# Optimization experiments

Measured on AMD Instinct MI355X. Metric: run time of the kernel, lower is better.

## Reference

```python
import jax, jax.numpy as jnp
import numpy as np

B, C, Ci, H, W = 4, 256, 128, 64, 64  # batch, in_channels, inter_channels, spatial
BN_EPS = 1e-5


def setup_inputs() -> dict:
    key = jax.random.key(0)
    ks = jax.random.split(key, 8)
    s = (2.0 / C) ** 0.5  # kaiming fan_in std for 1x1 conv over C inputs
    return {
        "a": jax.random.normal(ks[0], (B, C, H, W), jnp.float32),
        "b": jax.random.normal(ks[1], (B, C, H, W), jnp.float32),
        "theta_w": jax.random.normal(ks[2], (Ci, C), jnp.float32) * s,
        "theta_b": jnp.zeros((Ci,), jnp.float32),
        "phi_w": jax.random.normal(ks[3], (Ci, C), jnp.float32) * s,
        "phi_b": jnp.zeros((Ci,), jnp.float32),
        "g_w": jax.random.normal(ks[4], (Ci, C), jnp.float32) * s,
        "g_b": jnp.zeros((Ci,), jnp.float32),
        "W_w": jax.random.normal(ks[5], (C, Ci), jnp.float32) * (2.0 / Ci) ** 0.5,
        "bn_gamma": jnp.ones((C,), jnp.float32),
        "bn_beta": jnp.zeros((C,), jnp.float32),
        "bn_mean": jnp.zeros((C,), jnp.float32),
        "bn_var": jnp.ones((C,), jnp.float32),
    }


def _conv1x1(x, w, bias=None):
    # x: [B,Cin,H,W], w: [Cout,Cin] -> [B,Cout,H,W]
    y = jnp.einsum("oc,bchw->bohw", w, x)
    if bias is not None:
        y = y + bias[None, :, None, None]
    return y


def reference(a, b, theta_w, theta_b, phi_w, phi_b, g_w, g_b, W_w,
              bn_gamma, bn_beta, bn_mean, bn_var):
    Bsz, _, h, w = a.shape
    n = h * w
    theta_a = _conv1x1(a, theta_w, theta_b).reshape(Bsz, Ci, n).transpose(0, 2, 1)  # [B,N,Ci]
    phi_b_ = _conv1x1(b, phi_w, phi_b).reshape(Bsz, Ci, n)                          # [B,Ci,N]
    f = jnp.einsum("bnc,bcm->bnm", theta_a, phi_b_) / n                             # [B,N,N]
    g_b_ = _conv1x1(b, g_w, g_b).reshape(Bsz, Ci, n).transpose(0, 2, 1)             # [B,N,Ci]
    y = jnp.einsum("bnm,bmc->bnc", f, g_b_)                                         # [B,N,Ci]
    y = y.transpose(0, 2, 1).reshape(Bsz, Ci, h, w)
    wy = _conv1x1(y, W_w)                                                           # no bias
    inv = jax.lax.rsqrt(bn_var + BN_EPS)
    out = (wy - bn_mean[None, :, None, None]) * (bn_gamma * inv)[None, :, None, None] \
          + bn_beta[None, :, None, None]
    return out
```

## Files before the change

kernel.cpp:

```cpp
#include <hip/hip_runtime.h>
#include <hip/hip_bf16.h>

#define NSP 4096
#define CCH 256
#define CIN 128
#define BN_EPS 1e-5f

typedef __bf16 bf16x8 __attribute__((ext_vector_type(8)));
typedef __bf16 bf16x4 __attribute__((ext_vector_type(4)));
typedef float f32x4 __attribute__((ext_vector_type(4)));
typedef unsigned short u16x8 __attribute__((ext_vector_type(8)));


__device__ __forceinline__ float4 fetch_tr(const float* __restrict__ A, int lda, int m0,
                                           int k0, int tid) {
  const int r = tid >> 2, kq = (tid & 3) << 2;
  return *(const float4*)(A + (size_t)(m0 + r) * lda + k0 + kq);
}
__device__ __forceinline__ void stash_tr(float (*As)[68], float4 v, int tid) {
  const int r = tid >> 2, kq = (tid & 3) << 2;
  As[kq + 0][r] = v.x; As[kq + 1][r] = v.y; As[kq + 2][r] = v.z; As[kq + 3][r] = v.w;
}
__device__ __forceinline__ float4 fetch_dir(const float* __restrict__ B, int ldb, int k0,
                                            int n0, int tid) {
  const int kr = tid >> 4, nq = (tid & 15) << 2;
  return *(const float4*)(B + (size_t)(k0 + kr) * ldb + n0 + nq);
}
__device__ __forceinline__ void stash_dir(float (*Bs)[68], float4 v, int tid) {
  const int kr = tid >> 4, nq = (tid & 15) << 2;
  *(float4*)(&Bs[kr][nq]) = v;
}

__device__ __forceinline__ void mm16(const float (*As)[68], const float (*Bs)[68],
                                     float acc[4][4], int ty, int tx) {
#pragma unroll
  for (int kk = 0; kk < 16; ++kk) {
    const float4 av = *(const float4*)(&As[kk][ty << 2]);
    const float4 bv = *(const float4*)(&Bs[kk][tx << 2]);
    const float ar[4] = {av.x, av.y, av.z, av.w};
    const float br[4] = {bv.x, bv.y, bv.z, bv.w};
#pragma unroll
    for (int i = 0; i < 4; ++i)
#pragma unroll
      for (int j = 0; j < 4; ++j) acc[i][j] += ar[i] * br[j];
  }
}

__device__ __forceinline__ float wave_reduce(float v) {
#pragma unroll
  for (int off = 32; off; off >>= 1) v += __shfl_down(v, off);
  return v;
}

__device__ __forceinline__ void f8_hilo(const float* __restrict__ p,
                                        bf16x8& h, bf16x8& l) {
  const float4 v0 = *(const float4*)p;
  const float4 v1 = *(const float4*)(p + 4);
  const float vv[8] = {v0.x, v0.y, v0.z, v0.w, v1.x, v1.y, v1.z, v1.w};
  u16x8 hu, lu;
#pragma unroll
  for (int e = 0; e < 8; ++e) {
    const unsigned u = __float_as_uint(vv[e]);
    hu[e] = (unsigned short)(u >> 16);
    const float hf = __uint_as_float(u & 0xffff0000u);
    lu[e] = (unsigned short)(__float_as_uint(vv[e] - hf) >> 16);
  }
  h = *(bf16x8*)&hu;
  l = *(bf16x8*)&lu;
}

__global__ __launch_bounds__(256) void front_kernel(
    const float* __restrict__ bin, const float* __restrict__ a,
    const float* __restrict__ W_w, const float* __restrict__ g_w,
    const float* __restrict__ phi_w, const float* __restrict__ theta_w,
    const float* __restrict__ phi_b, const float* __restrict__ theta_b,
    const float* __restrict__ g_b,
    float* __restrict__ Gpart, float* __restrict__ srow,
    float* __restrict__ Wg, __bf16* __restrict__ Wghi, __bf16* __restrict__ Wglo,
    __bf16* __restrict__ PTthi, __bf16* __restrict__ PTtlo,
    __bf16* __restrict__ at,
    float* __restrict__ vb_g, float* __restrict__ vpt, float* __restrict__ wgb,
    float* __restrict__ dvec) {
  __shared__ float smem[64 * 68];
  const int idx = blockIdx.x;
  const int t = threadIdx.x;
  const int wave = t >> 6, lane = t & 63;
  if (idx < 1024) {
    const int jt = idx & 3, it = (idx >> 2) & 3;
    const int z = idx >> 4, batch = z >> 4, kc = z & 15;
    const int m = lane & 15, q = lane >> 4;
    const float* base = bin + (size_t)batch * CCH * NSP;
    const float* arow = base + (size_t)(it * 64 + wave * 16 + m) * NSP + kc * 256 + q * 8;
    const float* brow = base + (size_t)(jt * 64 + m) * NSP + kc * 256 + q * 8;
    f32x4 acc[4] = {};
#pragma unroll
    for (int ks = 0; ks < 8; ++ks) {
      const int k = ks * 32;
      bf16x8 ah, al;
      f8_hilo(arow + k, ah, al);
#pragma unroll
      for (int t4 = 0; t4 < 4; ++t4) {
        bf16x8 bh, bl;
        f8_hilo(brow + (size_t)t4 * 16 * NSP + k, bh, bl);
        acc[t4] = __builtin_amdgcn_mfma_f32_16x16x32_bf16(ah, bh, acc[t4], 0, 0, 0);
        acc[t4] = __builtin_amdgcn_mfma_f32_16x16x32_bf16(ah, bl, acc[t4], 0, 0, 0);
        acc[t4] = __builtin_amdgcn_mfma_f32_16x16x32_bf16(al, bh, acc[t4], 0, 0, 0);
      }
    }
    float* Gp = Gpart + ((size_t)(kc * 4 + batch)) * 65536;
#pragma unroll
    for (int t4 = 0; t4 < 4; ++t4)
#pragma unroll
      for (int r = 0; r < 4; ++r)
        Gp[(size_t)(it * 64 + wave * 16 + q * 4 + r) * 256 + jt * 64 + t4 * 16 + m] =
            acc[t4][r];
  } else if (idx < 2048) {
    const int p = idx - 1024;
    const int n0 = (p & 63) * 64, c0 = ((p >> 6) & 3) * 64, b = p >> 8;
    float (*tile)[68] = (float(*)[68])smem;
    const int cr = t >> 4, nq = (t & 15) << 2;
    const float* src = a + ((size_t)(b * CCH + c0)) * NSP + n0;
#pragma unroll
    for (int s = 0; s < 4; ++s) {
      const float4 v = *(const float4*)(src + (size_t)(cr + s * 16) * NSP + nq);
      *(float4*)&tile[cr + s * 16][nq] = v;
    }
    __syncthreads();
    const int n = t >> 2, cq = (t & 3) << 4;
    __bf16 outv[16];
#pragma unroll
    for (int i = 0; i < 16; ++i) outv[i] = (__bf16)tile[cq + i][n];
    __bf16* dst = at + ((size_t)(b * NSP + n0 + n)) * CCH + c0 + cq;
    *(bf16x8*)dst = *(bf16x8*)&outv[0];
    *(bf16x8*)(dst + 8) = *(bf16x8*)&outv[8];
  } else if (idx < 3072) {
    const int row = idx - 2048;
    const float* src = bin + (size_t)row * NSP + t * 16;
    float sum = 0.f;
#pragma unroll
    for (int i = 0; i < 4; ++i) {
      const float4 v = *(const float4*)(src + i * 4);
      sum += v.x + v.y + v.z + v.w;
    }
#pragma unroll
    for (int off = 32; off; off >>= 1) sum += __shfl_down(sum, off);
    if ((t & 63) == 0) smem[t >> 6] = sum;
    __syncthreads();
    if (t == 0) srow[row] = smem[0] + smem[1] + smem[2] + smem[3];
  } else if (idx < 3104) {
    const int p = idx - 3072;
    const int zsel = p >> 4, rem = p & 15;
    const int m0 = (rem >> 2) * 64, n0 = (rem & 3) * 64;
    float (*As)[68] = (float(*)[68])smem;
    float (*Bs)[68] = (float(*)[68])(smem + 16 * 68);
    const int ty = t >> 4, tx = t & 15;
    float acc[4][4] = {};
    if (zsel == 0) {
      float4 ar = fetch_tr(W_w, CIN, m0, 0, t);
      float4 br = fetch_dir(g_w, CCH, 0, n0, t);
      for (int kt = 0; kt < 8; ++kt) {
        stash_tr(As, ar, t); stash_dir(Bs, br, t);
        __syncthreads();
        if (kt < 7) { ar = fetch_tr(W_w, CIN, m0, (kt + 1) * 16, t);
                      br = fetch_dir(g_w, CCH, (kt + 1) * 16, n0, t); }
        mm16(As, Bs, acc, ty, tx);
        __syncthreads();
      }
#pragma unroll
      for (int i = 0; i < 4; ++i) {
        const size_t off = (size_t)(m0 + (ty << 2) + i) * 256 + n0 + (tx << 2);
        *(float4*)(Wg + off) = make_float4(acc[i][0], acc[i][1], acc[i][2], acc[i][3]);
        __bf16 h4[4], l4[4];
#pragma unroll
        for (int j = 0; j < 4; ++j) {
          const __bf16 h = (__bf16)acc[i][j];
          h4[j] = h; l4[j] = (__bf16)(acc[i][j] - (float)h);
        }
        *(bf16x4*)(Wghi + off) = *(bf16x4*)h4;
        *(bf16x4*)(Wglo + off) = *(bf16x4*)l4;
      }
    } else {
      float4 ar = fetch_dir(theta_w, CCH, 0, m0, t);
      float4 br = fetch_dir(phi_w, CCH, 0, n0, t);
      for (int kt = 0; kt < 8; ++kt) {
        stash_dir(As, ar, t); stash_dir(Bs, br, t);
        __syncthreads();
        if (kt < 7) { ar = fetch_dir(theta_w, CCH, (kt + 1) * 16, m0, t);
                      br = fetch_dir(phi_w, CCH, (kt + 1) * 16, n0, t); }
        mm16(As, Bs, acc, ty, tx);
        __syncthreads();
      }
#pragma unroll
      for (int i = 0; i < 4; ++i) {
        const size_t off = (size_t)(m0 + (ty << 2) + i) * 256 + n0 + (tx << 2);
        __bf16 h4[4], l4[4];
#pragma unroll
        for (int j = 0; j < 4; ++j) {
          const __bf16 h = (__bf16)acc[i][j];
          h4[j] = h; l4[j] = (__bf16)(acc[i][j] - (float)h);
        }
        *(bf16x4*)(PTthi + off) = *(bf16x4*)h4;
        *(bf16x4*)(PTtlo + off) = *(bf16x4*)l4;
      }
    }
  } else if (idx == 3104) {
    float* tb_s = smem;
    float* pb_s = smem + 128;
    if (t < 128) { tb_s[t] = theta_b[t]; pb_s[t] = phi_b[t]; }
    __syncthreads();
    float acc = 0.f;
#pragma unroll 8
    for (int i = 0; i < 128; ++i) acc += phi_w[(size_t)i * 256 + t] * tb_s[i];
    vb_g[t] = acc;
    if (t < 64) {
      float pv = pb_s[t] * tb_s[t] + pb_s[t + 64] * tb_s[t + 64];
      pv = wave_reduce(pv);
      if (t == 0) dvec[0] = pv;
    }
  } else if (idx == 3105) {
    float* pb_s = smem;
    if (t < 128) pb_s[t] = phi_b[t];
    __syncthreads();
    float acc = 0.f;
#pragma unroll 8
    for (int i = 0; i < 128; ++i) acc += pb_s[i] * theta_w[(size_t)i * 256 + t];
    vpt[t] = acc;
  } else {
    const int p = idx - 3106;
    float* gb_s = smem;
    if (t < 128) gb_s[t] = g_b[t];
    __syncthreads();
    const float2 gv = *(const float2*)&gb_s[lane * 2];
    for (int i = 0; i < 16; ++i) {
      const int o = p * 64 + wave * 16 + i;
      const float2 r = *(const float2*)(W_w + (size_t)o * 128 + lane * 2);
      float v = fmaf(r.x, gv.x, r.y * gv.y);
      v = wave_reduce(v);
      if (lane == 0) wgb[o] = v;
    }
  }
}

__global__ __launch_bounds__(256) void redw2_kernel(
    const float* __restrict__ Gpart, const float* __restrict__ vb_g,
    float* __restrict__ t2_g, const float* __restrict__ srow,
    const float* __restrict__ Wg,
    const __bf16* __restrict__ Wghi, const __bf16* __restrict__ Wglo,
    const __bf16* __restrict__ PTthi, const __bf16* __restrict__ PTtlo,
    __bf16* __restrict__ W2hi, __bf16* __restrict__ W2lo,
    float* __restrict__ Wgs, float* __restrict__ sPTv, float* __restrict__ dvec) {
  const int blk = blockIdx.x;
  const int t = threadIdx.x;
  const int wave = t >> 6, lane = t & 63;
  __shared__ __bf16 Gsh[16][264], Gsl[16][264];
  __shared__ float lds[256];
  if (blk < 256) {
    const int b = blk >> 6, rem = blk & 63;
    const int nt = rem >> 2, mt4 = rem & 3;
    const int rr = t >> 4;
    const int c0 = (t & 15) * 16;
    f32x4 s[4] = {};
#pragma unroll
    for (int p = 0; p < 16; ++p) {
      const float* src = Gpart + (((size_t)(p * 4 + b)) << 16) +
                         (size_t)(nt * 16 + rr) * 256 + c0;
#pragma unroll
      for (int e = 0; e < 4; ++e) s[e] += *(const f32x4*)(src + e * 4);
    }
    if (mt4 == 0) {
      float part = 0.f;
#pragma unroll
      for (int e = 0; e < 4; ++e) {
        const float4 vv = *(const float4*)(vb_g + c0 + e * 4);
        part += s[e][0] * vv.x + s[e][1] * vv.y + s[e][2] * vv.z + s[e][3] * vv.w;
      }
#pragma unroll
      for (int off = 8; off; off >>= 1) part += __shfl_down(part, off);
      if ((t & 15) == 0) t2_g[b * 256 + nt * 16 + rr] = part;
    }
    __bf16 h8[16], l8[16];
#pragma unroll
    for (int e = 0; e < 16; ++e) {
      const float x = s[e >> 2][e & 3];
      const __bf16 h = (__bf16)x;
      h8[e] = h; l8[e] = (__bf16)(x - (float)h);
    }
    *(bf16x8*)&Gsh[rr][c0] = *(bf16x8*)&h8[0];
    *(bf16x8*)&Gsh[rr][c0 + 8] = *(bf16x8*)&h8[8];
    *(bf16x8*)&Gsl[rr][c0] = *(bf16x8*)&l8[0];
    *(bf16x8*)&Gsl[rr][c0 + 8] = *(bf16x8*)&l8[8];
    __syncthreads();
    const int mt = mt4 * 4 + wave;
    const int m = lane & 15, q = lane >> 4;
    const __bf16* ah_p = Wghi + (size_t)(mt * 16 + m) * 256;
    const __bf16* al_p = Wglo + (size_t)(mt * 16 + m) * 256;
    f32x4 acc = {};
#pragma unroll
    for (int ks = 0; ks < 8; ++ks) {
      const int k = ks * 32 + q * 8;
      const bf16x8 bh = *(const bf16x8*)&Gsh[m][k];
      const bf16x8 bl = *(const bf16x8*)&Gsl[m][k];
      const bf16x8 ah = *(const bf16x8*)(ah_p + k);
      const bf16x8 al = *(const bf16x8*)(al_p + k);
      acc = __builtin_amdgcn_mfma_f32_16x16x32_bf16(ah, bh, acc, 0, 0, 0);
      acc = __builtin_amdgcn_mfma_f32_16x16x32_bf16(ah, bl, acc, 0, 0, 0);
      acc = __builtin_amdgcn_mfma_f32_16x16x32_bf16(al, bh, acc, 0, 0, 0);
    }
#pragma unroll
    for (int r = 0; r < 4; ++r) {
      const size_t off = ((size_t)b << 16) + (size_t)(mt * 16 + q * 4 + r) * 256 +
                         nt * 16 + m;
      const float v = acc[r];
      const __bf16 h = (__bf16)v;
      W2hi[off] = h;
      W2lo[off] = (__bf16)(v - (float)h);
    }
  } else {
    const int p = blk - 256;
    const int b = p >> 4, seg = p & 15;
    lds[t] = srow[b * 256 + t];
    __syncthreads();
    const float4 sv = *(const float4*)&lds[lane * 4];
    for (int i = wave; i < 16; i += 4) {
      const int o = seg * 16 + i;
      const float4 r = *(const float4*)(Wg + (size_t)o * 256 + lane * 4);
      float v = fmaf(r.x, sv.x, fmaf(r.y, sv.y, fmaf(r.z, sv.z, r.w * sv.w)));
      v = wave_reduce(v);
      if (lane == 0) Wgs[b * 256 + o] = v;
    }
    for (int i = wave; i < 16; i += 4) {
      const int c = seg * 16 + i;
      const bf16x4 ph = *(const bf16x4*)(PTthi + (size_t)c * 256 + lane * 4);
      const bf16x4 pl = *(const bf16x4*)(PTtlo + (size_t)c * 256 + lane * 4);
      const float svv[4] = {sv.x, sv.y, sv.z, sv.w};
      float v = 0.f;
#pragma unroll
      for (int e = 0; e < 4; ++e) v += ((float)ph[e] + (float)pl[e]) * svv[e];
      v = wave_reduce(v);
      if (lane == 0) sPTv[b * 256 + c] = v;
    }
    if (seg == 0 && wave == 0) {
      const float4 vbv = *(const float4*)(vb_g + lane * 4);
      float v = fmaf(vbv.x, sv.x, fmaf(vbv.y, sv.y, fmaf(vbv.z, sv.z, vbv.w * sv.w)));
      v = wave_reduce(v);
      if (lane == 0) dvec[1 + b] = v;
    }
  }
}

__global__ __launch_bounds__(256) void wout_mfma_kernel(
    const __bf16* __restrict__ W2hi, const __bf16* __restrict__ W2lo,
    const __bf16* __restrict__ PTthi, const __bf16* __restrict__ PTtlo,
    const float* __restrict__ Wgs, const float* __restrict__ sPT,
    const float* __restrict__ wgb, const float* __restrict__ vpt,
    const float* __restrict__ Wg, const float* __restrict__ t2_g,
    const float* __restrict__ dvec,
    const float* __restrict__ bn_gamma, const float* __restrict__ bn_beta,
    const float* __restrict__ bn_mean, const float* __restrict__ bn_var,
    __bf16* __restrict__ Whi, __bf16* __restrict__ Wlo,
    float* __restrict__ bias_out) {
  const int blk = blockIdx.x;
  const int t = threadIdx.x;
  const int wave = t >> 6, lane = t & 63;
  if (blk < 256) {
    const int tile = blk * 4 + wave;
    const int batch = tile >> 8, rem = tile & 255;
    const int mt = rem >> 4, nt = rem & 15;
    const int m = lane & 15, q = lane >> 4;
    const __bf16* ah_p = W2hi + (size_t)batch * 65536 + (size_t)(mt * 16 + m) * 256;
    const __bf16* al_p = W2lo + (size_t)batch * 65536 + (size_t)(mt * 16 + m) * 256;
    const __bf16* bh_p = PTthi + (size_t)(nt * 16 + m) * 256;
    const __bf16* bl_p = PTtlo + (size_t)(nt * 16 + m) * 256;
    f32x4 acc = {};
#pragma unroll
    for (int ks = 0; ks < 8; ++ks) {
      const int k = ks * 32 + q * 8;
      const bf16x8 ah = *(const bf16x8*)(ah_p + k);
      const bf16x8 al = *(const bf16x8*)(al_p + k);
      const bf16x8 bh = *(const bf16x8*)(bh_p + k);
      const bf16x8 bl = *(const bf16x8*)(bl_p + k);
      acc = __builtin_amdgcn_mfma_f32_16x16x32_bf16(ah, bh, acc, 0, 0, 0);
      acc = __builtin_amdgcn_mfma_f32_16x16x32_bf16(ah, bl, acc, 0, 0, 0);
      acc = __builtin_amdgcn_mfma_f32_16x16x32_bf16(al, bh, acc, 0, 0, 0);
    }
    const float invN = 1.0f / 4096.0f;
    const int c = nt * 16 + m;
    const float vpt_c = vpt[c];
    const float sPT_c = sPT[batch * 256 + c];
#pragma unroll
    for (int r = 0; r < 4; ++r) {
      const int o = mt * 16 + q * 4 + r;
      const float sc = bn_gamma[o] * rsqrtf(bn_var[o] + BN_EPS);
      const float w = sc * ((acc[r] + Wgs[batch * 256 + o] * vpt_c + wgb[o] * sPT_c) * invN +
                            wgb[o] * vpt_c);
      const size_t off = (size_t)batch * 65536 + (size_t)o * 256 + c;
      const __bf16 h = (__bf16)w;
      Whi[off] = h;
      Wlo[off] = (__bf16)(w - (float)h);
    }
  } else {
    const int p = blk - 256;
    const int b = p >> 2, quarter = p & 3;
    __shared__ float t2s[256];
    t2s[t] = t2_g[b * 256 + t];
    __syncthreads();
    const float d1 = dvec[0], d2 = dvec[1 + b];
    const float invN = 1.0f / 4096.0f;
    const float4 tv = *(const float4*)&t2s[lane * 4];
    for (int it = 0; it < 16; ++it) {
      const int o = quarter * 64 + wave * 16 + it;
      const float4 r = *(const float4*)(Wg + (size_t)o * 256 + lane * 4);
      float v = fmaf(r.x, tv.x, fmaf(r.y, tv.y, fmaf(r.z, tv.z, r.w * tv.w)));
      v = wave_reduce(v);
      if (lane == 0) {
        const float bias_full = (v + Wgs[b * 256 + o] * d1 +
                                 wgb[o] * (d2 + 4096.0f * d1)) * invN;
        const float sc = bn_gamma[o] * rsqrtf(bn_var[o] + BN_EPS);
        bias_out[b * 256 + o] = sc * (bias_full - bn_mean[o]) + bn_beta[o];
      }
    }
  }
}

__global__ __launch_bounds__(256) void out_mfma_kernel(const __bf16* __restrict__ Whi,
                                                       const __bf16* __restrict__ Wlo,
                                                       const __bf16* __restrict__ at,
                                                       const float* __restrict__ bias_out,
                                                       float* __restrict__ out) {
  const int nt = blockIdx.x, mt = blockIdx.y, b = blockIdx.z;
  const int wave = threadIdx.x >> 6, lane = threadIdx.x & 63;
  const int m = lane & 15, q = lane >> 4;
  const int o = mt * 64 + wave * 16 + m;
  const __bf16* wh = Whi + (size_t)b * 65536 + (size_t)o * 256;
  const __bf16* wl = Wlo + (size_t)b * 65536 + (size_t)o * 256;
  const __bf16* atb = at + ((size_t)b * NSP + nt * 32) * CCH;
  f32x4 acc[2] = {};
#pragma unroll
  for (int ks = 0; ks < 8; ++ks) {
    const int k = ks * 32 + q * 8;
    const bf16x8 ah = *(const bf16x8*)(wh + k);
    const bf16x8 al = *(const bf16x8*)(wl + k);
#pragma unroll
    for (int t4 = 0; t4 < 2; ++t4) {
      const bf16x8 bh = *(const bf16x8*)(atb + (size_t)(t4 * 16 + m) * 256 + k);
      acc[t4] = __builtin_amdgcn_mfma_f32_16x16x32_bf16(ah, bh, acc[t4], 0, 0, 0);
      acc[t4] = __builtin_amdgcn_mfma_f32_16x16x32_bf16(al, bh, acc[t4], 0, 0, 0);
    }
  }
  float* ob = out + (size_t)b * CCH * NSP;
#pragma unroll
  for (int r = 0; r < 4; ++r) {
    const int orow = mt * 64 + wave * 16 + q * 4 + r;
    const float bo = bias_out[b * 256 + orow];
#pragma unroll
    for (int t4 = 0; t4 < 2; ++t4)
      ob[(size_t)orow * NSP + nt * 32 + t4 * 16 + m] = acc[t4][r] + bo;
  }
}

extern "C" void kernel_launch(void* const* d_in, const int* in_sizes, int n_in,
                              void* d_out, int out_size, void* d_ws, size_t ws_size,
                              hipStream_t stream) {
  (void)in_sizes; (void)n_in; (void)out_size; (void)ws_size;
  const float* a       = (const float*)d_in[0];
  const float* bI      = (const float*)d_in[1];
  const float* theta_w = (const float*)d_in[2];
  const float* theta_b = (const float*)d_in[3];
  const float* phi_w   = (const float*)d_in[4];
  const float* phi_b   = (const float*)d_in[5];
  const float* g_w     = (const float*)d_in[6];
  const float* g_b     = (const float*)d_in[7];
  const float* W_w     = (const float*)d_in[8];
  const float* bn_gamma= (const float*)d_in[9];
  const float* bn_beta = (const float*)d_in[10];
  const float* bn_mean = (const float*)d_in[11];
  const float* bn_var  = (const float*)d_in[12];
  float* out = (float*)d_out;
  float* ws  = (float*)d_ws;

  float* Gpart    = ws;
  float* srow     = ws + 4194304;
  float* Wg       = ws + 4195328;
  float* bias_out = ws + 4260864;
  float* Wgs      = ws + 4261888;
  float* sPTv     = ws + 4262912;
  float* wgb      = ws + 4263936;
  float* vpt      = ws + 4264192;
  float* vb_g     = ws + 4264448;
  float* t2_g     = ws + 4264704;
  float* dvec     = ws + 4265728;
  __bf16* at    = (__bf16*)(ws + 4265984);
  __bf16* Wghi  = (__bf16*)(ws + 6363136);
  __bf16* Wglo  = (__bf16*)(ws + 6395904);
  __bf16* PTthi = (__bf16*)(ws + 6428672);
  __bf16* PTtlo = (__bf16*)(ws + 6461440);
  __bf16* W2hi  = (__bf16*)(ws + 6494208);
  __bf16* W2lo  = (__bf16*)(ws + 6625280);
  __bf16* Whi   = (__bf16*)(ws + 6756352);
  __bf16* Wlo   = (__bf16*)(ws + 6887424);

  front_kernel<<<dim3(3110), dim3(256), 0, stream>>>(bI, a, W_w, g_w, phi_w, theta_w,
                                                     phi_b, theta_b, g_b,
                                                     Gpart, srow, Wg, Wghi, Wglo,
                                                     PTthi, PTtlo, at,
                                                     vb_g, vpt, wgb, dvec);
  redw2_kernel<<<dim3(320), dim3(256), 0, stream>>>(Gpart, vb_g, t2_g, srow, Wg,
                                                    Wghi, Wglo, PTthi, PTtlo,
                                                    W2hi, W2lo, Wgs, sPTv, dvec);
  wout_mfma_kernel<<<dim3(272), dim3(256), 0, stream>>>(W2hi, W2lo, PTthi, PTtlo,
                                                        Wgs, sPTv, wgb, vpt, Wg, t2_g,
                                                        dvec, bn_gamma, bn_beta, bn_mean,
                                                        bn_var, Whi, Wlo, bias_out);
  out_mfma_kernel<<<dim3(128, 4, 4), dim3(256), 0, stream>>>(Whi, Wlo, at, bias_out, out);
}
```

Measured before the change: 200.0 us.

## Pre-split b into bf16 hi/lo in a separate pass and enlarge per-block tiles

The bf16 hi/lo split of input b moves out of the Gram-matrix MFMA loop into a prep pass fused with the row-sum reduction. A new gram kernel then reads the pre-split bf16 data instead of converting fp32 values repeatedly. The redw2, wout and out kernels each compute four times or twice as many output tiles per block, reusing loaded operands with fewer blocks. This adds an extra kernel launch and hi/lo workspace traffic, and the larger tiles lower the block count, which can reduce occupancy.

```diff
diff --git a/kernel.cpp b/kernel.cpp
--- a/kernel.cpp
+++ b/kernel.cpp
@@ -52,30 +52,14 @@
   return v;
 }
 
-__device__ __forceinline__ void f8_hilo(const float* __restrict__ p,
-                                        bf16x8& h, bf16x8& l) {
-  const float4 v0 = *(const float4*)p;
-  const float4 v1 = *(const float4*)(p + 4);
-  const float vv[8] = {v0.x, v0.y, v0.z, v0.w, v1.x, v1.y, v1.z, v1.w};
-  u16x8 hu, lu;
-#pragma unroll
-  for (int e = 0; e < 8; ++e) {
-    const unsigned u = __float_as_uint(vv[e]);
-    hu[e] = (unsigned short)(u >> 16);
-    const float hf = __uint_as_float(u & 0xffff0000u);
-    lu[e] = (unsigned short)(__float_as_uint(vv[e] - hf) >> 16);
-  }
-  h = *(bf16x8*)&hu;
-  l = *(bf16x8*)&lu;
-}
-
-__global__ __launch_bounds__(256) void front_kernel(
+__global__ __launch_bounds__(256) void prep_kernel(
     const float* __restrict__ bin, const float* __restrict__ a,
     const float* __restrict__ W_w, const float* __restrict__ g_w,
     const float* __restrict__ phi_w, const float* __restrict__ theta_w,
     const float* __restrict__ phi_b, const float* __restrict__ theta_b,
     const float* __restrict__ g_b,
-    float* __restrict__ Gpart, float* __restrict__ srow,
+    __bf16* __restrict__ bhi, __bf16* __restrict__ blo,
+    float* __restrict__ srow,
     float* __restrict__ Wg, __bf16* __restrict__ Wghi, __bf16* __restrict__ Wglo,
     __bf16* __restrict__ PTthi, __bf16* __restrict__ PTtlo,
     __bf16* __restrict__ at,
@@ -86,34 +70,34 @@
   const int t = threadIdx.x;
   const int wave = t >> 6, lane = t & 63;
   if (idx < 1024) {
-    const int jt = idx & 3, it = (idx >> 2) & 3;
-    const int z = idx >> 4, batch = z >> 4, kc = z & 15;
-    const int m = lane & 15, q = lane >> 4;
-    const float* base = bin + (size_t)batch * CCH * NSP;
-    const float* arow = base + (size_t)(it * 64 + wave * 16 + m) * NSP + kc * 256 + q * 8;
-    const float* brow = base + (size_t)(jt * 64 + m) * NSP + kc * 256 + q * 8;
-    f32x4 acc[4] = {};
-#pragma unroll
-    for (int ks = 0; ks < 8; ++ks) {
-      const int k = ks * 32;
-      bf16x8 ah, al;
-      f8_hilo(arow + k, ah, al);
-#pragma unroll
-      for (int t4 = 0; t4 < 4; ++t4) {
-        bf16x8 bh, bl;
-        f8_hilo(brow + (size_t)t4 * 16 * NSP + k, bh, bl);
-        acc[t4] = __builtin_amdgcn_mfma_f32_16x16x32_bf16(ah, bh, acc[t4], 0, 0, 0);
-        acc[t4] = __builtin_amdgcn_mfma_f32_16x16x32_bf16(ah, bl, acc[t4], 0, 0, 0);
-        acc[t4] = __builtin_amdgcn_mfma_f32_16x16x32_bf16(al, bh, acc[t4], 0, 0, 0);
-      }
-    }
-    float* Gp = Gpart + ((size_t)(kc * 4 + batch)) * 65536;
-#pragma unroll
-    for (int t4 = 0; t4 < 4; ++t4)
-#pragma unroll
-      for (int r = 0; r < 4; ++r)
-        Gp[(size_t)(it * 64 + wave * 16 + q * 4 + r) * 256 + jt * 64 + t4 * 16 + m] =
-            acc[t4][r];
+    const int row = idx;
+    const float* src = bin + (size_t)row * NSP + t * 16;
+    float sum = 0.f;
+    unsigned short h16[16], l16[16];
+#pragma unroll
+    for (int i = 0; i < 4; ++i) {
+      const float4 v = *(const float4*)(src + i * 4);
+      const float vv[4] = {v.x, v.y, v.z, v.w};
+      sum += v.x + v.y + v.z + v.w;
+#pragma unroll
+      for (int e = 0; e < 4; ++e) {
+        const unsigned u = __float_as_uint(vv[e]);
+        h16[i * 4 + e] = (unsigned short)(u >> 16);
+        const float hf = __uint_as_float(u & 0xffff0000u);
+        l16[i * 4 + e] = (unsigned short)(__float_as_uint(vv[e] - hf) >> 16);
+      }
+    }
+    unsigned short* dh = (unsigned short*)bhi + (size_t)row * NSP + t * 16;
+    unsigned short* dl = (unsigned short*)blo + (size_t)row * NSP + t * 16;
+    *(u16x8*)dh = *(u16x8*)&h16[0];
+    *(u16x8*)(dh + 8) = *(u16x8*)&h16[8];
+    *(u16x8*)dl = *(u16x8*)&l16[0];
+    *(u16x8*)(dl + 8) = *(u16x8*)&l16[8];
+#pragma unroll
+    for (int off = 32; off; off >>= 1) sum += __shfl_down(sum, off);
+    if (lane == 0) smem[wave] = sum;
+    __syncthreads();
+    if (t == 0) srow[row] = smem[0] + smem[1] + smem[2] + smem[3];
   } else if (idx < 2048) {
     const int p = idx - 1024;
     const int n0 = (p & 63) * 64, c0 = ((p >> 6) & 3) * 64, b = p >> 8;
@@ -133,22 +117,8 @@
     __bf16* dst = at + ((size_t)(b * NSP + n0 + n)) * CCH + c0 + cq;
     *(bf16x8*)dst = *(bf16x8*)&outv[0];
     *(bf16x8*)(dst + 8) = *(bf16x8*)&outv[8];
-  } else if (idx < 3072) {
-    const int row = idx - 2048;
-    const float* src = bin + (size_t)row * NSP + t * 16;
-    float sum = 0.f;
-#pragma unroll
-    for (int i = 0; i < 4; ++i) {
-      const float4 v = *(const float4*)(src + i * 4);
-      sum += v.x + v.y + v.z + v.w;
-    }
-#pragma unroll
-    for (int off = 32; off; off >>= 1) sum += __shfl_down(sum, off);
-    if ((t & 63) == 0) smem[t >> 6] = sum;
-    __syncthreads();
-    if (t == 0) srow[row] = smem[0] + smem[1] + smem[2] + smem[3];
-  } else if (idx < 3104) {
-    const int p = idx - 3072;
+  } else if (idx < 2080) {
+    const int p = idx - 2048;
     const int zsel = p >> 4, rem = p & 15;
     const int m0 = (rem >> 2) * 64, n0 = (rem & 3) * 64;
     float (*As)[68] = (float(*)[68])smem;
@@ -203,7 +173,7 @@
         *(bf16x4*)(PTtlo + off) = *(bf16x4*)l4;
       }
     }
-  } else if (idx == 3104) {
+  } else if (idx == 2080) {
     float* tb_s = smem;
     float* pb_s = smem + 128;
     if (t < 128) { tb_s[t] = theta_b[t]; pb_s[t] = phi_b[t]; }
@@ -217,7 +187,7 @@
       pv = wave_reduce(pv);
       if (t == 0) dvec[0] = pv;
     }
-  } else if (idx == 3105) {
+  } else if (idx == 2081) {
     float* pb_s = smem;
     if (t < 128) pb_s[t] = phi_b[t];
     __syncthreads();
@@ -226,7 +196,7 @@
     for (int i = 0; i < 128; ++i) acc += pb_s[i] * theta_w[(size_t)i * 256 + t];
     vpt[t] = acc;
   } else {
-    const int p = idx - 3106;
+    const int p = idx - 2082;
     float* gb_s = smem;
     if (t < 128) gb_s[t] = g_b[t];
     __syncthreads();
@@ -239,6 +209,44 @@
       if (lane == 0) wgb[o] = v;
     }
   }
+}
+
+__global__ __launch_bounds__(256) void gram_kernel(
+    const __bf16* __restrict__ bhi, const __bf16* __restrict__ blo,
+    float* __restrict__ Gpart) {
+  const int idx = blockIdx.x;
+  const int t = threadIdx.x;
+  const int wave = t >> 6, lane = t & 63;
+  const int jt = idx & 3, it = (idx >> 2) & 3;
+  const int z = idx >> 4, batch = z >> 4, kc = z & 15;
+  const int m = lane & 15, q = lane >> 4;
+  const size_t base = (size_t)batch * CCH * NSP;
+  const __bf16* ah_p = bhi + base + (size_t)(it * 64 + wave * 16 + m) * NSP + kc * 256 + q * 8;
+  const __bf16* al_p = blo + base + (size_t)(it * 64 + wave * 16 + m) * NSP + kc * 256 + q * 8;
+  const __bf16* bh_p = bhi + base + (size_t)(jt * 64 + m) * NSP + kc * 256 + q * 8;
+  const __bf16* bl_p = blo + base + (size_t)(jt * 64 + m) * NSP + kc * 256 + q * 8;
+  f32x4 acc[4] = {};
+#pragma unroll
+  for (int ks = 0; ks < 8; ++ks) {
+    const int k = ks * 32;
+    const bf16x8 ah = *(const bf16x8*)(ah_p + k);
+    const bf16x8 al = *(const bf16x8*)(al_p + k);
+#pragma unroll
+    for (int t4 = 0; t4 < 4; ++t4) {
+      const bf16x8 bh = *(const bf16x8*)(bh_p + (size_t)t4 * 16 * NSP + k);
+      const bf16x8 bl = *(const bf16x8*)(bl_p + (size_t)t4 * 16 * NSP + k);
+      acc[t4] = __builtin_amdgcn_mfma_f32_16x16x32_bf16(ah, bh, acc[t4], 0, 0, 0);
+      acc[t4] = __builtin_amdgcn_mfma_f32_16x16x32_bf16(ah, bl, acc[t4], 0, 0, 0);
+      acc[t4] = __builtin_amdgcn_mfma_f32_16x16x32_bf16(al, bh, acc[t4], 0, 0, 0);
+    }
+  }
+  float* Gp = Gpart + ((size_t)(kc * 4 + batch)) * 65536;
+#pragma unroll
+  for (int t4 = 0; t4 < 4; ++t4)
+#pragma unroll
+    for (int r = 0; r < 4; ++r)
+      Gp[(size_t)(it * 64 + wave * 16 + q * 4 + r) * 256 + jt * 64 + t4 * 16 + m] =
+          acc[t4][r];
 }
 
 __global__ __launch_bounds__(256) void redw2_kernel(
@@ -254,9 +262,8 @@
   const int wave = t >> 6, lane = t & 63;
   __shared__ __bf16 Gsh[16][264], Gsl[16][264];
   __shared__ float lds[256];
-  if (blk < 256) {
-    const int b = blk >> 6, rem = blk & 63;
-    const int nt = rem >> 2, mt4 = rem & 3;
+  if (blk < 64) {
+    const int b = blk >> 4, nt = blk & 15;
     const int rr = t >> 4;
     const int c0 = (t & 15) * 16;
     f32x4 s[4] = {};
@@ -267,7 +274,7 @@
 #pragma unroll
       for (int e = 0; e < 4; ++e) s[e] += *(const f32x4*)(src + e * 4);
     }
-    if (mt4 == 0) {
+    {
       float part = 0.f;
 #pragma unroll
       for (int e = 0; e < 4; ++e) {
@@ -290,33 +297,38 @@
     *(bf16x8*)&Gsl[rr][c0] = *(bf16x8*)&l8[0];
     *(bf16x8*)&Gsl[rr][c0 + 8] = *(bf16x8*)&l8[8];
     __syncthreads();
-    const int mt = mt4 * 4 + wave;
     const int m = lane & 15, q = lane >> 4;
-    const __bf16* ah_p = Wghi + (size_t)(mt * 16 + m) * 256;
-    const __bf16* al_p = Wglo + (size_t)(mt * 16 + m) * 256;
-    f32x4 acc = {};
+    f32x4 acc[4] = {};
 #pragma unroll
     for (int ks = 0; ks < 8; ++ks) {
       const int k = ks * 32 + q * 8;
       const bf16x8 bh = *(const bf16x8*)&Gsh[m][k];
       const bf16x8 bl = *(const bf16x8*)&Gsl[m][k];
-      const bf16x8 ah = *(const bf16x8*)(ah_p + k);
-      const bf16x8 al = *(const bf16x8*)(al_p + k);
-      acc = __builtin_amdgcn_mfma_f32_16x16x32_bf16(ah, bh, acc, 0, 0, 0);
-      acc = __builtin_amdgcn_mfma_f32_16x16x32_bf16(ah, bl, acc, 0, 0, 0);
-      acc = __builtin_amdgcn_mfma_f32_16x16x32_bf16(al, bh, acc, 0, 0, 0);
-    }
-#pragma unroll
-    for (int r = 0; r < 4; ++r) {
-      const size_t off = ((size_t)b << 16) + (size_t)(mt * 16 + q * 4 + r) * 256 +
-                         nt * 16 + m;
-      const float v = acc[r];
-      const __bf16 h = (__bf16)v;
-      W2hi[off] = h;
-      W2lo[off] = (__bf16)(v - (float)h);
+#pragma unroll
+      for (int i = 0; i < 4; ++i) {
+        const int mt = i * 4 + wave;
+        const bf16x8 ah = *(const bf16x8*)(Wghi + (size_t)(mt * 16 + m) * 256 + k);
+        const bf16x8 al = *(const bf16x8*)(Wglo + (size_t)(mt * 16 + m) * 256 + k);
+        acc[i] = __builtin_amdgcn_mfma_f32_16x16x32_bf16(ah, bh, acc[i], 0, 0, 0);
+        acc[i] = __builtin_amdgcn_mfma_f32_16x16x32_bf16(ah, bl, acc[i], 0, 0, 0);
+        acc[i] = __builtin_amdgcn_mfma_f32_16x16x32_bf16(al, bh, acc[i], 0, 0, 0);
+      }
+    }
+#pragma unroll
+    for (int i = 0; i < 4; ++i) {
+      const int mt = i * 4 + wave;
+#pragma unroll
+      for (int r = 0; r < 4; ++r) {
+        const size_t off = ((size_t)b << 16) + (size_t)(mt * 16 + q * 4 + r) * 256 +
+                           nt * 16 + m;
+        const float v = acc[i][r];
+        const __bf16 h = (__bf16)v;
+        W2hi[off] = h;
+        W2lo[off] = (__bf16)(v - (float)h);
+      }
     }
   } else {
-    const int p = blk - 256;
+    const int p = blk - 64;
     const int b = p >> 4, seg = p & 15;
     lds[t] = srow[b * 256 + t];
     __syncthreads();
@@ -362,44 +374,50 @@
   const int blk = blockIdx.x;
   const int t = threadIdx.x;
   const int wave = t >> 6, lane = t & 63;
-  if (blk < 256) {
-    const int tile = blk * 4 + wave;
-    const int batch = tile >> 8, rem = tile & 255;
-    const int mt = rem >> 4, nt = rem & 15;
+  if (blk < 64) {
+    const int batch = blk >> 4, nt = blk & 15;
     const int m = lane & 15, q = lane >> 4;
-    const __bf16* ah_p = W2hi + (size_t)batch * 65536 + (size_t)(mt * 16 + m) * 256;
-    const __bf16* al_p = W2lo + (size_t)batch * 65536 + (size_t)(mt * 16 + m) * 256;
     const __bf16* bh_p = PTthi + (size_t)(nt * 16 + m) * 256;
     const __bf16* bl_p = PTtlo + (size_t)(nt * 16 + m) * 256;
-    f32x4 acc = {};
+    const __bf16* w2h = W2hi + (size_t)batch * 65536;
+    const __bf16* w2l = W2lo + (size_t)batch * 65536;
+    f32x4 acc[4] = {};
 #pragma unroll
     for (int ks = 0; ks < 8; ++ks) {
       const int k = ks * 32 + q * 8;
-      const bf16x8 ah = *(const bf16x8*)(ah_p + k);
-      const bf16x8 al = *(const bf16x8*)(al_p + k);
       const bf16x8 bh = *(const bf16x8*)(bh_p + k);
       const bf16x8 bl = *(const bf16x8*)(bl_p + k);
-      acc = __builtin_amdgcn_mfma_f32_16x16x32_bf16(ah, bh, acc, 0, 0, 0);
-      acc = __builtin_amdgcn_mfma_f32_16x16x32_bf16(ah, bl, acc, 0, 0, 0);
-      acc = __builtin_amdgcn_mfma_f32_16x16x32_bf16(al, bh, acc, 0, 0, 0);
+#pragma unroll
+      for (int i = 0; i < 4; ++i) {
+        const int mt = i * 4 + wave;
+        const bf16x8 ah = *(const bf16x8*)(w2h + (size_t)(mt * 16 + m) * 256 + k);
+        const bf16x8 al = *(const bf16x8*)(w2l + (size_t)(mt * 16 + m) * 256 + k);
+        acc[i] = __builtin_amdgcn_mfma_f32_16x16x32_bf16(ah, bh, acc[i], 0, 0, 0);
+        acc[i] = __builtin_amdgcn_mfma_f32_16x16x32_bf16(ah, bl, acc[i], 0, 0, 0);
+        acc[i] = __builtin_amdgcn_mfma_f32_16x16x32_bf16(al, bh, acc[i], 0, 0, 0);
+      }
     }
     const float invN = 1.0f / 4096.0f;
     const int c = nt * 16 + m;
     const float vpt_c = vpt[c];
     const float sPT_c = sPT[batch * 256 + c];
 #pragma unroll
-    for (int r = 0; r < 4; ++r) {
-      const int o = mt * 16 + q * 4 + r;
-      const float sc = bn_gamma[o] * rsqrtf(bn_var[o] + BN_EPS);
-      const float w = sc * ((acc[r] + Wgs[batch * 256 + o] * vpt_c + wgb[o] * sPT_c) * invN +
-                            wgb[o] * vpt_c);
-      const size_t off = (size_t)batch * 65536 + (size_t)o * 256 + c;
-      const __bf16 h = (__bf16)w;
-      Whi[off] = h;
-      Wlo[off] = (__bf16)(w - (float)h);
+    for (int i = 0; i < 4; ++i) {
+      const int mt = i * 4 + wave;
+#pragma unroll
+      for (int r = 0; r < 4; ++r) {
+        const int o = mt * 16 + q * 4 + r;
+        const float sc = bn_gamma[o] * rsqrtf(bn_var[o] + BN_EPS);
+        const float w = sc * ((acc[i][r] + Wgs[batch * 256 + o] * vpt_c + wgb[o] * sPT_c) * invN +
+                              wgb[o] * vpt_c);
+        const size_t off = (size_t)batch * 65536 + (size_t)o * 256 + c;
+        const __bf16 h = (__bf16)w;
+        Whi[off] = h;
+        Wlo[off] = (__bf16)(w - (float)h);
+      }
     }
   } else {
-    const int p = blk - 256;
+    const int p = blk - 64;
     const int b = p >> 2, quarter = p & 3;
     __shared__ float t2s[256];
     t2s[t] = t2_g[b * 256 + t];
@@ -433,15 +451,15 @@
   const int o = mt * 64 + wave * 16 + m;
   const __bf16* wh = Whi + (size_t)b * 65536 + (size_t)o * 256;
   const __bf16* wl = Wlo + (size_t)b * 65536 + (size_t)o * 256;
-  const __bf16* atb = at + ((size_t)b * NSP + nt * 32) * CCH;
-  f32x4 acc[2] = {};
+  const __bf16* atb = at + ((size_t)b * NSP + nt * 64) * CCH;
+  f32x4 acc[4] = {};
 #pragma unroll
   for (int ks = 0; ks < 8; ++ks) {
     const int k = ks * 32 + q * 8;
     const bf16x8 ah = *(const bf16x8*)(wh + k);
     const bf16x8 al = *(const bf16x8*)(wl + k);
 #pragma unroll
-    for (int t4 = 0; t4 < 2; ++t4) {
+    for (int t4 = 0; t4 < 4; ++t4) {
       const bf16x8 bh = *(const bf16x8*)(atb + (size_t)(t4 * 16 + m) * 256 + k);
       acc[t4] = __builtin_amdgcn_mfma_f32_16x16x32_bf16(ah, bh, acc[t4], 0, 0, 0);
       acc[t4] = __builtin_amdgcn_mfma_f32_16x16x32_bf16(al, bh, acc[t4], 0, 0, 0);
@@ -453,8 +471,8 @@
     const int orow = mt * 64 + wave * 16 + q * 4 + r;
     const float bo = bias_out[b * 256 + orow];
 #pragma unroll
-    for (int t4 = 0; t4 < 2; ++t4)
-      ob[(size_t)orow * NSP + nt * 32 + t4 * 16 + m] = acc[t4][r] + bo;
+    for (int t4 = 0; t4 < 4; ++t4)
+      ob[(size_t)orow * NSP + nt * 64 + t4 * 16 + m] = acc[t4][r] + bo;
   }
 }
 
@@ -498,18 +516,21 @@
   __bf16* W2lo  = (__bf16*)(ws + 6625280);
   __bf16* Whi   = (__bf16*)(ws + 6756352);
   __bf16* Wlo   = (__bf16*)(ws + 6887424);
-
-  front_kernel<<<dim3(3110), dim3(256), 0, stream>>>(bI, a, W_w, g_w, phi_w, theta_w,
-                                                     phi_b, theta_b, g_b,
-                                                     Gpart, srow, Wg, Wghi, Wglo,
-                                                     PTthi, PTtlo, at,
-                                                     vb_g, vpt, wgb, dvec);
-  redw2_kernel<<<dim3(320), dim3(256), 0, stream>>>(Gpart, vb_g, t2_g, srow, Wg,
+  __bf16* bhi   = (__bf16*)(ws + 7018496);
+  __bf16* blo   = (__bf16*)(ws + 9115648);
+
+  prep_kernel<<<dim3(2086), dim3(256), 0, stream>>>(bI, a, W_w, g_w, phi_w, theta_w,
+                                                    phi_b, theta_b, g_b,
+                                                    bhi, blo, srow, Wg, Wghi, Wglo,
+                                                    PTthi, PTtlo, at,
+                                                    vb_g, vpt, wgb, dvec);
+  gram_kernel<<<dim3(1024), dim3(256), 0, stream>>>(bhi, blo, Gpart);
+  redw2_kernel<<<dim3(128), dim3(256), 0, stream>>>(Gpart, vb_g, t2_g, srow, Wg,
                                                     Wghi, Wglo, PTthi, PTtlo,
                                                     W2hi, W2lo, Wgs, sPTv, dvec);
-  wout_mfma_kernel<<<dim3(272), dim3(256), 0, stream>>>(W2hi, W2lo, PTthi, PTtlo,
-                                                        Wgs, sPTv, wgb, vpt, Wg, t2_g,
-                                                        dvec, bn_gamma, bn_beta, bn_mean,
-                                                        bn_var, Whi, Wlo, bias_out);
-  out_mfma_kernel<<<dim3(128, 4, 4), dim3(256), 0, stream>>>(Whi, Wlo, at, bias_out, out);
-}
+  wout_mfma_kernel<<<dim3(80), dim3(256), 0, stream>>>(W2hi, W2lo, PTthi, PTtlo,
+                                                       Wgs, sPTv, wgb, vpt, Wg, t2_g,
+                                                       dvec, bn_gamma, bn_beta, bn_mean,
+                                                       bn_var, Whi, Wlo, bias_out);
+  out_mfma_kernel<<<dim3(64, 4, 4), dim3(256), 0, stream>>>(Whi, Wlo, at, bias_out, out);
+}
```

Result: no change. 203.6 us (+1.8%).
